# Optimization experiments

Measured on AMD Instinct MI355X. Metric: run time of the kernel, lower is better.

Reference implementation:

```python
import jax, jax.numpy as jnp
import numpy as np

B = 128            # fixed by min(128, len(sample)) loop
NODES_PER_GRAPH = 100
N_NODES = B * NODES_PER_GRAPH
HID = 512          # args.num_hidden
EMB = 1024         # pretrained embedding dim (t_linear in_features)
TWEET_VOCAB = 300000
DESC_VOCAB = 150000
EPS = 1e-5


def setup_inputs() -> dict:
    key = jax.random.key(0)
    ks = jax.random.split(key, 12)
    sample = jnp.stack([
        jax.random.randint(ks[0], (B,), 0, DESC_VOCAB),
        jax.random.randint(ks[1], (B,), 0, TWEET_VOCAB),
        jax.random.randint(ks[2], (B,), 0, DESC_VOCAB),
    ], axis=1)  # [B,3] int
    # sorted node->graph assignment; every graph has >=2 nodes so u_idx+1 is valid
    graph_batch = jnp.repeat(jnp.arange(B), NODES_PER_GRAPH)  # [N_NODES]
    p_feature = jax.random.normal(ks[3], (N_NODES, HID), dtype=jnp.float32)
    tweet_emb = jax.random.normal(ks[4], (TWEET_VOCAB, EMB), dtype=jnp.float32) * 0.02
    desc_emb = jax.random.normal(ks[5], (DESC_VOCAB, EMB), dtype=jnp.float32) * 0.02
    t_w = jax.random.normal(ks[6], (HID, EMB), dtype=jnp.float32) / np.sqrt(EMB)
    t_b = jnp.zeros((HID,), dtype=jnp.float32)
    w1 = jax.random.normal(ks[7], (256, 3 * HID), dtype=jnp.float32) / np.sqrt(3 * HID)
    b1 = jnp.zeros((256,), dtype=jnp.float32)
    gamma = jnp.ones((256,), dtype=jnp.float32)
    beta = jnp.zeros((256,), dtype=jnp.float32)
    w2 = jax.random.normal(ks[8], (1, 256), dtype=jnp.float32) / np.sqrt(256)
    b2 = jnp.zeros((1,), dtype=jnp.float32)
    return {"sample": sample, "graph_batch": graph_batch, "p_feature": p_feature,
            "tweet_emb": tweet_emb, "desc_emb": desc_emb, "t_w": t_w, "t_b": t_b,
            "w1": w1, "b1": b1, "gamma": gamma, "beta": beta, "w2": w2, "b2": b2}


def reference(sample, graph_batch, p_feature, tweet_emb, desc_emb,
              t_w, t_b, w1, b1, gamma, beta, w2, b2):
    # torch.nonzero(batch == i)[0] -> first node index of graph i;
    # graph_batch is sorted, so this is a searchsorted (replaces the 128-iter loop)
    u_idx = jnp.searchsorted(graph_batch, jnp.arange(B))  # [B]
    v_idx = u_idx + 1
    u_feat = p_feature[u_idx]  # [B, HID]
    v_feat = p_feature[v_idx]  # [B, HID]

    t = lambda e: e @ t_w.T + t_b  # Linear(1024 -> HID)
    inp = jnp.concatenate([
        u_feat + t(desc_emb[sample[:, 0]]),
        t(tweet_emb[sample[:, 1]]),
        v_feat + t(desc_emb[sample[:, 2]]),
    ], axis=1)  # [B, 3*HID]

    h = inp @ w1.T + b1  # [B, 256]
    # BatchNorm1d in training mode: biased batch statistics
    mu = jnp.mean(h, axis=0)
    var = jnp.mean((h - mu) ** 2, axis=0)
    h = (h - mu) * jax.lax.rsqrt(var + EPS) * gamma + beta
    # Dropout treated as identity (eval / deterministic reference)
    h = jax.nn.relu(h)
    return jax.nn.sigmoid(h @ w2.T + b2)  # [B, 1]
```

## Files before the change

### kernel.cpp

```cpp
#include <hip/hip_runtime.h>
#include <math.h>

#define HID 512
#define EMB 1024
#define N1 1536
#define N2 256
#define P2S (128 * 256)

typedef __attribute__((ext_vector_type(8))) __bf16 bf16x8;
typedef __attribute__((ext_vector_type(4))) __bf16 bf16x4;
typedef __attribute__((ext_vector_type(4))) float fx4;

#define OFF_ABUF 0
#define OFF_TWB  786432
#define OFF_INPB 1835008
#define OFF_P2   2228224
#define OFF_UIDX 2490368

__device__ __forceinline__ fx4 mfma16(bf16x8 a, bf16x8 b, fx4 c) {
    return __builtin_amdgcn_mfma_f32_16x16x32_bf16(a, b, c, 0, 0, 0);
}

__device__ __forceinline__ bf16x8 cvt8(float4 a, float4 b) {
    bf16x8 r;
    r[0] = (__bf16)a.x; r[1] = (__bf16)a.y; r[2] = (__bf16)a.z; r[3] = (__bf16)a.w;
    r[4] = (__bf16)b.x; r[5] = (__bf16)b.y; r[6] = (__bf16)b.z; r[7] = (__bf16)b.w;
    return r;
}

__global__ __launch_bounds__(256)
void kPrep(const int* __restrict__ sample, const int* __restrict__ gb, int n_nodes,
           const float* __restrict__ tweet_emb, const float* __restrict__ desc_emb,
           const float* __restrict__ t_w,
           __bf16* __restrict__ Abuf, __bf16* __restrict__ twb,
           int* __restrict__ uidx)
{
    const int blk = blockIdx.x;
    const int t   = threadIdx.x;

    if (blk < 384) {
        const int s = blk >> 7, b = blk & 127;
        const int id = sample[b * 3 + s];
        const float* src = (s == 1) ? (tweet_emb + (size_t)id * EMB)
                                    : (desc_emb + (size_t)id * EMB);
        float4 v = *(const float4*)(src + t * 4);
        bf16x4 o = {(__bf16)v.x, (__bf16)v.y, (__bf16)v.z, (__bf16)v.w};
        *(bf16x4*)(Abuf + (size_t)blk * EMB + t * 4) = o;
    } else if (blk < 896) {
        const int r = blk - 384;
        float4 v = *(const float4*)(t_w + (size_t)r * EMB + t * 4);
        bf16x4 o = {(__bf16)v.x, (__bf16)v.y, (__bf16)v.z, (__bf16)v.w};
        *(bf16x4*)(twb + (size_t)r * EMB + t * 4) = o;
    } else {
        const int n = (blk - 896) * 256 + t;
        if (n < n_nodes) {
            const int g = gb[n];
            if (n == 0 || gb[n - 1] != g) uidx[g] = n;
        }
    }
}

__global__ __launch_bounds__(256, 1)
void kG1(const __bf16* __restrict__ Abuf, const __bf16* __restrict__ twb,
         const float* __restrict__ t_b, const float* __restrict__ p_feature,
         const int* __restrict__ uidx, __bf16* __restrict__ inp_bf)
{
    const int n0 = blockIdx.x * 32;
    const int m0 = blockIdx.y * 32;
    const int t  = threadIdx.x;
    const int wid = t >> 6, l = t & 63;
    const int mbase = (wid >> 1) * 16, nbase = (wid & 1) * 16;

    __shared__ __bf16 Alds[32 * 1024];
    __shared__ __bf16 Blds[32 * 1024];

    bf16x8 areg[16], breg[16];
    #pragma unroll
    for (int i = 0; i < 16; ++i) {
        const int c = i * 256 + t;
        const int row = c >> 7, g = c & 127;
        areg[i] = *(const bf16x8*)(Abuf + (size_t)(m0 + row) * EMB + g * 8);
        breg[i] = *(const bf16x8*)(twb  + (size_t)(n0 + row) * EMB + g * 8);
    }
    #pragma unroll
    for (int i = 0; i < 16; ++i) {
        const int c = i * 256 + t;
        const int row = c >> 7, g = c & 127;
        const int gp = g ^ (row & 7);
        *(bf16x8*)(Alds + row * 1024 + gp * 8) = areg[i];
        *(bf16x8*)(Blds + row * 1024 + gp * 8) = breg[i];
    }
    __syncthreads();

    fx4 acc0 = {}, acc1 = {};
    const int fr = l & 15, fq = l >> 4;
    const __bf16* Ab = Alds + (mbase + fr) * 1024;
    const __bf16* Bb = Blds + (nbase + fr) * 1024;
    const int ax = (mbase + fr) & 7, bx = (nbase + fr) & 7;
    #pragma unroll
    for (int s = 0; s < 32; s += 2) {
        bf16x8 a0 = *(const bf16x8*)(Ab + ((s * 4 + fq) ^ ax) * 8);
        bf16x8 b0 = *(const bf16x8*)(Bb + ((s * 4 + fq) ^ bx) * 8);
        acc0 = mfma16(a0, b0, acc0);
        bf16x8 a1 = *(const bf16x8*)(Ab + (((s + 1) * 4 + fq) ^ ax) * 8);
        bf16x8 b1 = *(const bf16x8*)(Bb + (((s + 1) * 4 + fq) ^ bx) * 8);
        acc1 = mfma16(a1, b1, acc1);
    }

    const int sid  = m0 >> 7;
    const int col  = n0 + nbase + fr;
    const int row0 = m0 + mbase + fq * 4;
    const float tb = t_b[col];
    #pragma unroll
    for (int j = 0; j < 4; ++j) {
        const int r = row0 + j;
        float v = acc0[j] + acc1[j] + tb;
        if (sid != 1) {
            const int node = uidx[r & 127] + ((sid == 2) ? 1 : 0);
            v += p_feature[(size_t)node * HID + col];
        }
        inp_bf[(size_t)(r & 127) * N1 + sid * HID + col] = (__bf16)v;
    }
}

__global__ __launch_bounds__(256, 1)
void kG2(const __bf16* __restrict__ inp_bf, const float* __restrict__ w1,
         float* __restrict__ part2)
{
    const int n0 = blockIdx.x * 32;
    const int m0 = blockIdx.y * 32;
    const int ks = blockIdx.z;
    const int t  = threadIdx.x;
    const int wid = t >> 6, l = t & 63;
    const int mbase = (wid >> 1) * 16, nbase = (wid & 1) * 16;

    __shared__ __bf16 Alds[32 * 768];
    __shared__ __bf16 Blds[32 * 768];

    const int row = t >> 3;
    const int gt  = t & 7;

    bf16x8 areg[12];
    const __bf16* abase = inp_bf + (size_t)(m0 + row) * N1 + ks * 768;
    #pragma unroll
    for (int j = 0; j < 12; ++j)
        areg[j] = *(const bf16x8*)(abase + (gt + j * 8) * 8);

    float4 br[24];
    const float* bbase = w1 + (size_t)(n0 + row) * N1 + ks * 768;
    #pragma unroll
    for (int j = 0; j < 12; ++j) {
        br[2 * j]     = *(const float4*)(bbase + (gt + j * 8) * 8);
        br[2 * j + 1] = *(const float4*)(bbase + (gt + j * 8) * 8 + 4);
    }
    #pragma unroll
    for (int j = 0; j < 12; ++j) {
        const int g  = gt + j * 8;
        const int gp = g ^ (row & 7);
        *(bf16x8*)(Alds + row * 768 + gp * 8) = areg[j];
        *(bf16x8*)(Blds + row * 768 + gp * 8) = cvt8(br[2 * j], br[2 * j + 1]);
    }
    __syncthreads();

    fx4 acc0 = {}, acc1 = {};
    const int fr = l & 15, fq = l >> 4;
    const __bf16* Ab = Alds + (mbase + fr) * 768;
    const __bf16* Bb = Blds + (nbase + fr) * 768;
    const int ax = (mbase + fr) & 7, bx = (nbase + fr) & 7;
    #pragma unroll
    for (int s = 0; s < 24; s += 2) {
        bf16x8 a0 = *(const bf16x8*)(Ab + ((s * 4 + fq) ^ ax) * 8);
        bf16x8 b0 = *(const bf16x8*)(Bb + ((s * 4 + fq) ^ bx) * 8);
        acc0 = mfma16(a0, b0, acc0);
        bf16x8 a1 = *(const bf16x8*)(Ab + (((s + 1) * 4 + fq) ^ ax) * 8);
        bf16x8 b1 = *(const bf16x8*)(Bb + (((s + 1) * 4 + fq) ^ bx) * 8);
        acc1 = mfma16(a1, b1, acc1);
    }

    float* dst = part2 + (size_t)ks * P2S;
    const int col  = n0 + nbase + fr;
    const int row0 = m0 + mbase + fq * 4;
    #pragma unroll
    for (int j = 0; j < 4; ++j)
        dst[(size_t)(row0 + j) * N2 + col] = acc0[j] + acc1[j];
}

__global__ __launch_bounds__(256)
void kEF(const float* __restrict__ part2, const float* __restrict__ b1,
         const float* __restrict__ gamma, const float* __restrict__ beta,
         const float* __restrict__ w2, const float* __restrict__ b2,
         float* __restrict__ out)
{
    __shared__ float s_scale[256];
    __shared__ float s_shift[256];
    const int t = threadIdx.x;

    const float bias = b1[t];
    float sum = 0.f, sq = 0.f;
    #pragma unroll 8
    for (int r = 0; r < 128; ++r) {
        float v = part2[r * N2 + t] + part2[P2S + r * N2 + t] + bias;
        sum += v;
        sq  += v * v;
    }
    const float mu  = sum * (1.0f / 128.0f);
    const float var = sq * (1.0f / 128.0f) - mu * mu;
    const float rs  = rsqrtf(var + 1e-5f);
    const float sc  = gamma[t] * rs;
    s_scale[t] = sc;
    s_shift[t] = beta[t] - mu * sc;
    __syncthreads();

    const int wv = t >> 6, l = t & 63;
    #pragma unroll
    for (int rr = 0; rr < 2; ++rr) {
        const int b = blockIdx.x * 8 + wv * 2 + rr;
        float acc = 0.f;
        #pragma unroll
        for (int i = 0; i < 4; ++i) {
            const int j = l + i * 64;
            float v = part2[b * N2 + j] + part2[P2S + b * N2 + j] + b1[j];
            float x = v * s_scale[j] + s_shift[j];
            x = fmaxf(x, 0.f);
            acc += x * w2[j];
        }
        #pragma unroll
        for (int off = 32; off; off >>= 1) acc += __shfl_xor(acc, off);
        if (l == 0) out[b] = 1.0f / (1.0f + expf(-(acc + b2[0])));
    }
}

extern "C" void kernel_launch(void* const* d_in, const int* in_sizes, int n_in,
                              void* d_out, int out_size, void* d_ws, size_t ws_size,
                              hipStream_t stream) {
    const int*   sample    = (const int*)  d_in[0];
    const int*   gb        = (const int*)  d_in[1];
    const float* p_feature = (const float*)d_in[2];
    const float* tweet_emb = (const float*)d_in[3];
    const float* desc_emb  = (const float*)d_in[4];
    const float* t_w       = (const float*)d_in[5];
    const float* t_b       = (const float*)d_in[6];
    const float* w1        = (const float*)d_in[7];
    const float* b1        = (const float*)d_in[8];
    const float* gamma     = (const float*)d_in[9];
    const float* beta      = (const float*)d_in[10];
    const float* w2        = (const float*)d_in[11];
    const float* b2        = (const float*)d_in[12];
    float* out = (float*)d_out;

    char* ws = (char*)d_ws;
    __bf16* Abuf   = (__bf16*)(ws + OFF_ABUF);
    __bf16* twb    = (__bf16*)(ws + OFF_TWB);
    __bf16* inp_bf = (__bf16*)(ws + OFF_INPB);
    float*  part2  = (float*)(ws + OFF_P2);
    int*    uidx   = (int*)  (ws + OFF_UIDX);

    const int n_nodes = in_sizes[1];
    const int scatter_blocks = (n_nodes + 255) / 256;

    kPrep<<<896 + scatter_blocks, 256, 0, stream>>>(sample, gb, n_nodes,
        tweet_emb, desc_emb, t_w, Abuf, twb, uidx);
    kG1<<<dim3(16, 12), 256, 0, stream>>>(Abuf, twb, t_b, p_feature, uidx, inp_bf);
    kG2<<<dim3(8, 4, 2), 256, 0, stream>>>(inp_bf, w1, part2);
    kEF<<<16, 256, 0, stream>>>(part2, b1, gamma, beta, w2, b2, out);
}
```

Before: 28.83 us.

## Fuse embedding gather, weight conversion and graph-start search into first GEMM

Removes the separate prep kernel. The first GEMM kernel now gathers the fp32 embedding rows and t_w rows itself, converts them to bf16 in registers, and finds graph start nodes by scanning graph_batch into shared memory. This saves a launch and the bf16 round-trip through global memory. In exchange, each block reads fp32 data (twice the bytes), t_w rows are re-read by all 12 row-blocks, and every non-tweet block scans the full graph_batch array.

```diff
diff --git a/kernel.cpp b/kernel.cpp
--- a/kernel.cpp
+++ b/kernel.cpp
@@ -8,14 +8,10 @@
 #define P2S (128 * 256)
 
 typedef __attribute__((ext_vector_type(8))) __bf16 bf16x8;
-typedef __attribute__((ext_vector_type(4))) __bf16 bf16x4;
 typedef __attribute__((ext_vector_type(4))) float fx4;
 
-#define OFF_ABUF 0
-#define OFF_TWB  786432
-#define OFF_INPB 1835008
-#define OFF_P2   2228224
-#define OFF_UIDX 2490368
+#define OFF_INPB 0
+#define OFF_P2   393216
 
 __device__ __forceinline__ fx4 mfma16(bf16x8 a, bf16x8 b, fx4 c) {
     return __builtin_amdgcn_mfma_f32_16x16x32_bf16(a, b, c, 0, 0, 0);
@@ -28,67 +24,64 @@
     return r;
 }
 
-__global__ __launch_bounds__(256)
-void kPrep(const int* __restrict__ sample, const int* __restrict__ gb, int n_nodes,
-           const float* __restrict__ tweet_emb, const float* __restrict__ desc_emb,
-           const float* __restrict__ t_w,
-           __bf16* __restrict__ Abuf, __bf16* __restrict__ twb,
-           int* __restrict__ uidx)
-{
-    const int blk = blockIdx.x;
-    const int t   = threadIdx.x;
-
-    if (blk < 384) {
-        const int s = blk >> 7, b = blk & 127;
-        const int id = sample[b * 3 + s];
-        const float* src = (s == 1) ? (tweet_emb + (size_t)id * EMB)
-                                    : (desc_emb + (size_t)id * EMB);
-        float4 v = *(const float4*)(src + t * 4);
-        bf16x4 o = {(__bf16)v.x, (__bf16)v.y, (__bf16)v.z, (__bf16)v.w};
-        *(bf16x4*)(Abuf + (size_t)blk * EMB + t * 4) = o;
-    } else if (blk < 896) {
-        const int r = blk - 384;
-        float4 v = *(const float4*)(t_w + (size_t)r * EMB + t * 4);
-        bf16x4 o = {(__bf16)v.x, (__bf16)v.y, (__bf16)v.z, (__bf16)v.w};
-        *(bf16x4*)(twb + (size_t)r * EMB + t * 4) = o;
-    } else {
-        const int n = (blk - 896) * 256 + t;
-        if (n < n_nodes) {
-            const int g = gb[n];
-            if (n == 0 || gb[n - 1] != g) uidx[g] = n;
-        }
-    }
-}
-
 __global__ __launch_bounds__(256, 1)
-void kG1(const __bf16* __restrict__ Abuf, const __bf16* __restrict__ twb,
-         const float* __restrict__ t_b, const float* __restrict__ p_feature,
-         const int* __restrict__ uidx, __bf16* __restrict__ inp_bf)
+void kG1(const int* __restrict__ sample, const int* __restrict__ gb, int n_nodes,
+         const float* __restrict__ p_feature,
+         const float* __restrict__ tweet_emb, const float* __restrict__ desc_emb,
+         const float* __restrict__ t_w, const float* __restrict__ t_b,
+         __bf16* __restrict__ inp_bf)
 {
     const int n0 = blockIdx.x * 32;
     const int m0 = blockIdx.y * 32;
+    const int sid = m0 >> 7;
+    const int b0  = m0 & 127;
     const int t  = threadIdx.x;
     const int wid = t >> 6, l = t & 63;
     const int mbase = (wid >> 1) * 16, nbase = (wid & 1) * 16;
 
     __shared__ __bf16 Alds[32 * 1024];
     __shared__ __bf16 Blds[32 * 1024];
+    __shared__ int node_lds[32];
+
+    if (sid != 1) {
+        for (int n = t; n < n_nodes; n += 256) {
+            const int g = gb[n];
+            const int rel = g - b0;
+            if (rel >= 0 && rel < 32) {
+                if (n == 0 || gb[n - 1] != g) node_lds[rel] = n;
+            }
+        }
+    }
+
+    const int row = t >> 3;
+    const int gt  = t & 7;
+
+    const int bb  = b0 + row;
+    const int id  = sample[bb * 3 + sid];
+    const float* erow = ((sid == 1) ? tweet_emb : desc_emb) + (size_t)id * EMB;
+    const float* wrow = t_w + (size_t)(n0 + row) * EMB;
 
     bf16x8 areg[16], breg[16];
     #pragma unroll
-    for (int i = 0; i < 16; ++i) {
-        const int c = i * 256 + t;
-        const int row = c >> 7, g = c & 127;
-        areg[i] = *(const bf16x8*)(Abuf + (size_t)(m0 + row) * EMB + g * 8);
-        breg[i] = *(const bf16x8*)(twb  + (size_t)(n0 + row) * EMB + g * 8);
-    }
-    #pragma unroll
-    for (int i = 0; i < 16; ++i) {
-        const int c = i * 256 + t;
-        const int row = c >> 7, g = c & 127;
+    for (int j = 0; j < 16; ++j) {
+        const int g = gt + j * 8;
+        float4 a0 = *(const float4*)(erow + g * 8);
+        float4 a1 = *(const float4*)(erow + g * 8 + 4);
+        areg[j] = cvt8(a0, a1);
+    }
+    #pragma unroll
+    for (int j = 0; j < 16; ++j) {
+        const int g = gt + j * 8;
+        float4 c0 = *(const float4*)(wrow + g * 8);
+        float4 c1 = *(const float4*)(wrow + g * 8 + 4);
+        breg[j] = cvt8(c0, c1);
+    }
+    #pragma unroll
+    for (int j = 0; j < 16; ++j) {
+        const int g  = gt + j * 8;
         const int gp = g ^ (row & 7);
-        *(bf16x8*)(Alds + row * 1024 + gp * 8) = areg[i];
-        *(bf16x8*)(Blds + row * 1024 + gp * 8) = breg[i];
+        *(bf16x8*)(Alds + row * 1024 + gp * 8) = areg[j];
+        *(bf16x8*)(Blds + row * 1024 + gp * 8) = breg[j];
     }
     __syncthreads();
 
@@ -107,19 +100,18 @@
         acc1 = mfma16(a1, b1, acc1);
     }
 
-    const int sid  = m0 >> 7;
     const int col  = n0 + nbase + fr;
-    const int row0 = m0 + mbase + fq * 4;
+    const int roff = mbase + fq * 4;
     const float tb = t_b[col];
     #pragma unroll
     for (int j = 0; j < 4; ++j) {
-        const int r = row0 + j;
+        const int b = b0 + roff + j;
         float v = acc0[j] + acc1[j] + tb;
         if (sid != 1) {
-            const int node = uidx[r & 127] + ((sid == 2) ? 1 : 0);
+            const int node = node_lds[roff + j] + ((sid == 2) ? 1 : 0);
             v += p_feature[(size_t)node * HID + col];
         }
-        inp_bf[(size_t)(r & 127) * N1 + sid * HID + col] = (__bf16)v;
+        inp_bf[(size_t)b * N1 + sid * HID + col] = (__bf16)v;
     }
 }
 
@@ -249,18 +241,12 @@
     float* out = (float*)d_out;
 
     char* ws = (char*)d_ws;
-    __bf16* Abuf   = (__bf16*)(ws + OFF_ABUF);
-    __bf16* twb    = (__bf16*)(ws + OFF_TWB);
     __bf16* inp_bf = (__bf16*)(ws + OFF_INPB);
     float*  part2  = (float*)(ws + OFF_P2);
-    int*    uidx   = (int*)  (ws + OFF_UIDX);
-
     const int n_nodes = in_sizes[1];
-    const int scatter_blocks = (n_nodes + 255) / 256;
-
-    kPrep<<<896 + scatter_blocks, 256, 0, stream>>>(sample, gb, n_nodes,
-        tweet_emb, desc_emb, t_w, Abuf, twb, uidx);
-    kG1<<<dim3(16, 12), 256, 0, stream>>>(Abuf, twb, t_b, p_feature, uidx, inp_bf);
+
+    kG1<<<dim3(16, 12), 256, 0, stream>>>(sample, gb, n_nodes, p_feature,
+                                          tweet_emb, desc_emb, t_w, t_b, inp_bf);
     kG2<<<dim3(8, 4, 2), 256, 0, stream>>>(inp_bf, w1, part2);
     kEF<<<16, 256, 0, stream>>>(part2, b1, gamma, beta, w2, b2, out);
 }
```

After: 34.13 us. 1.18x slower.

## Pre-convert w1 to bf16 in prep kernel and split kG2 K-dimension four ways

Applied to the files above, without the earlier changes.

The fp32-to-bf16 conversion of w1 moves out of the GEMM2 kernel and into the prep kernel, using 256 extra blocks. kG2 now loads bf16 directly and splits K into 4 slices instead of 2, giving 128 blocks with half the shared memory and no occupancy cap. The epilogue kernel sums four partial buffers instead of two. The intent is to shorten kG2's load-bound critical path and raise parallelism, at the cost of an extra w1b write/read and more partial-sum traffic.

```diff
diff --git a/kernel.cpp b/kernel.cpp
--- a/kernel.cpp
+++ b/kernel.cpp
@@ -13,27 +13,21 @@
 
 #define OFF_ABUF 0
 #define OFF_TWB  786432
-#define OFF_INPB 1835008
-#define OFF_P2   2228224
-#define OFF_UIDX 2490368
+#define OFF_W1B  1835008
+#define OFF_INPB 2621440
+#define OFF_P2   3014656
+#define OFF_UIDX 3538944
 
 __device__ __forceinline__ fx4 mfma16(bf16x8 a, bf16x8 b, fx4 c) {
     return __builtin_amdgcn_mfma_f32_16x16x32_bf16(a, b, c, 0, 0, 0);
-}
-
-__device__ __forceinline__ bf16x8 cvt8(float4 a, float4 b) {
-    bf16x8 r;
-    r[0] = (__bf16)a.x; r[1] = (__bf16)a.y; r[2] = (__bf16)a.z; r[3] = (__bf16)a.w;
-    r[4] = (__bf16)b.x; r[5] = (__bf16)b.y; r[6] = (__bf16)b.z; r[7] = (__bf16)b.w;
-    return r;
 }
 
 __global__ __launch_bounds__(256)
 void kPrep(const int* __restrict__ sample, const int* __restrict__ gb, int n_nodes,
            const float* __restrict__ tweet_emb, const float* __restrict__ desc_emb,
-           const float* __restrict__ t_w,
+           const float* __restrict__ t_w, const float* __restrict__ w1,
            __bf16* __restrict__ Abuf, __bf16* __restrict__ twb,
-           int* __restrict__ uidx)
+           __bf16* __restrict__ w1b, int* __restrict__ uidx)
 {
     const int blk = blockIdx.x;
     const int t   = threadIdx.x;
@@ -51,8 +45,16 @@
         float4 v = *(const float4*)(t_w + (size_t)r * EMB + t * 4);
         bf16x4 o = {(__bf16)v.x, (__bf16)v.y, (__bf16)v.z, (__bf16)v.w};
         *(bf16x4*)(twb + (size_t)r * EMB + t * 4) = o;
+    } else if (blk < 1152) {
+        const int r = blk - 896;
+        #pragma unroll
+        for (int i = t; i < 384; i += 256) {
+            float4 v = *(const float4*)(w1 + (size_t)r * N1 + i * 4);
+            bf16x4 o = {(__bf16)v.x, (__bf16)v.y, (__bf16)v.z, (__bf16)v.w};
+            *(bf16x4*)(w1b + (size_t)r * N1 + i * 4) = o;
+        }
     } else {
-        const int n = (blk - 896) * 256 + t;
+        const int n = (blk - 1152) * 256 + t;
         if (n < n_nodes) {
             const int g = gb[n];
             if (n == 0 || gb[n - 1] != g) uidx[g] = n;
@@ -123,8 +125,8 @@
     }
 }
 
-__global__ __launch_bounds__(256, 1)
-void kG2(const __bf16* __restrict__ inp_bf, const float* __restrict__ w1,
+__global__ __launch_bounds__(256)
+void kG2(const __bf16* __restrict__ inp_bf, const __bf16* __restrict__ w1b,
          float* __restrict__ part2)
 {
     const int n0 = blockIdx.x * 32;
@@ -134,41 +136,34 @@
     const int wid = t >> 6, l = t & 63;
     const int mbase = (wid >> 1) * 16, nbase = (wid & 1) * 16;
 
-    __shared__ __bf16 Alds[32 * 768];
-    __shared__ __bf16 Blds[32 * 768];
-
-    const int row = t >> 3;
-    const int gt  = t & 7;
-
-    bf16x8 areg[12];
-    const __bf16* abase = inp_bf + (size_t)(m0 + row) * N1 + ks * 768;
-    #pragma unroll
-    for (int j = 0; j < 12; ++j)
-        areg[j] = *(const bf16x8*)(abase + (gt + j * 8) * 8);
-
-    float4 br[24];
-    const float* bbase = w1 + (size_t)(n0 + row) * N1 + ks * 768;
-    #pragma unroll
-    for (int j = 0; j < 12; ++j) {
-        br[2 * j]     = *(const float4*)(bbase + (gt + j * 8) * 8);
-        br[2 * j + 1] = *(const float4*)(bbase + (gt + j * 8) * 8 + 4);
-    }
-    #pragma unroll
-    for (int j = 0; j < 12; ++j) {
-        const int g  = gt + j * 8;
+    __shared__ __bf16 Alds[32 * 384];
+    __shared__ __bf16 Blds[32 * 384];
+
+    bf16x8 areg[6], breg[6];
+    #pragma unroll
+    for (int i = 0; i < 6; ++i) {
+        const int c = i * 256 + t;
+        const int row = c / 48, g = c % 48;
+        areg[i] = *(const bf16x8*)(inp_bf + (size_t)(m0 + row) * N1 + ks * 384 + g * 8);
+        breg[i] = *(const bf16x8*)(w1b   + (size_t)(n0 + row) * N1 + ks * 384 + g * 8);
+    }
+    #pragma unroll
+    for (int i = 0; i < 6; ++i) {
+        const int c = i * 256 + t;
+        const int row = c / 48, g = c % 48;
         const int gp = g ^ (row & 7);
-        *(bf16x8*)(Alds + row * 768 + gp * 8) = areg[j];
-        *(bf16x8*)(Blds + row * 768 + gp * 8) = cvt8(br[2 * j], br[2 * j + 1]);
+        *(bf16x8*)(Alds + row * 384 + gp * 8) = areg[i];
+        *(bf16x8*)(Blds + row * 384 + gp * 8) = breg[i];
     }
     __syncthreads();
 
     fx4 acc0 = {}, acc1 = {};
     const int fr = l & 15, fq = l >> 4;
-    const __bf16* Ab = Alds + (mbase + fr) * 768;
-    const __bf16* Bb = Blds + (nbase + fr) * 768;
+    const __bf16* Ab = Alds + (mbase + fr) * 384;
+    const __bf16* Bb = Blds + (nbase + fr) * 384;
     const int ax = (mbase + fr) & 7, bx = (nbase + fr) & 7;
     #pragma unroll
-    for (int s = 0; s < 24; s += 2) {
+    for (int s = 0; s < 12; s += 2) {
         bf16x8 a0 = *(const bf16x8*)(Ab + ((s * 4 + fq) ^ ax) * 8);
         bf16x8 b0 = *(const bf16x8*)(Bb + ((s * 4 + fq) ^ bx) * 8);
         acc0 = mfma16(a0, b0, acc0);
@@ -197,9 +192,10 @@
 
     const float bias = b1[t];
     float sum = 0.f, sq = 0.f;
-    #pragma unroll 8
+    #pragma unroll 4
     for (int r = 0; r < 128; ++r) {
-        float v = part2[r * N2 + t] + part2[P2S + r * N2 + t] + bias;
+        float v = (((part2[r * N2 + t] + part2[P2S + r * N2 + t])
+                  + part2[2 * P2S + r * N2 + t]) + part2[3 * P2S + r * N2 + t]) + bias;
         sum += v;
         sq  += v * v;
     }
@@ -219,7 +215,8 @@
         #pragma unroll
         for (int i = 0; i < 4; ++i) {
             const int j = l + i * 64;
-            float v = part2[b * N2 + j] + part2[P2S + b * N2 + j] + b1[j];
+            float v = (((part2[b * N2 + j] + part2[P2S + b * N2 + j])
+                      + part2[2 * P2S + b * N2 + j]) + part2[3 * P2S + b * N2 + j]) + b1[j];
             float x = v * s_scale[j] + s_shift[j];
             x = fmaxf(x, 0.f);
             acc += x * w2[j];
@@ -251,6 +248,7 @@
     char* ws = (char*)d_ws;
     __bf16* Abuf   = (__bf16*)(ws + OFF_ABUF);
     __bf16* twb    = (__bf16*)(ws + OFF_TWB);
+    __bf16* w1b    = (__bf16*)(ws + OFF_W1B);
     __bf16* inp_bf = (__bf16*)(ws + OFF_INPB);
     float*  part2  = (float*)(ws + OFF_P2);
     int*    uidx   = (int*)  (ws + OFF_UIDX);
@@ -258,9 +256,9 @@
     const int n_nodes = in_sizes[1];
     const int scatter_blocks = (n_nodes + 255) / 256;
 
-    kPrep<<<896 + scatter_blocks, 256, 0, stream>>>(sample, gb, n_nodes,
-        tweet_emb, desc_emb, t_w, Abuf, twb, uidx);
+    kPrep<<<1152 + scatter_blocks, 256, 0, stream>>>(sample, gb, n_nodes,
+        tweet_emb, desc_emb, t_w, w1, Abuf, twb, w1b, uidx);
     kG1<<<dim3(16, 12), 256, 0, stream>>>(Abuf, twb, t_b, p_feature, uidx, inp_bf);
-    kG2<<<dim3(8, 4, 2), 256, 0, stream>>>(inp_bf, w1, part2);
+    kG2<<<dim3(8, 4, 4), 256, 0, stream>>>(inp_bf, w1b, part2);
     kEF<<<16, 256, 0, stream>>>(part2, b1, gamma, beta, w2, b2, out);
 }
```

Measured after the change: 34.17 us. 1.19x slower.
